# Kernel optimization log

Hardware: AMD Instinct MI355X
Metric: run time of the kernel (lower is better)

## Reference

```python
import jax, jax.numpy as jnp
import numpy as np

N = 2048       # num nodes
E = 4096       # num edges
D_NODE = 128
D_EDGE = 128
H = 4          # heads
DH = D_EDGE // H
C = 16         # num classes
NODE_K = N // 2   # node_k_ratio = 0.5
EDGE_K = E // 2   # edge_k_ratio = 0.5
NEG = -1e9


def setup_inputs() -> dict:
    key = jax.random.key(0)
    ks = jax.random.split(key, 16)
    w = lambda k, shape: jax.random.normal(k, shape, jnp.float32) * 0.02
    return {
        "node_features": jax.random.normal(ks[0], (N, D_NODE), jnp.float32),
        "edge_features": jax.random.normal(ks[1], (E, D_EDGE), jnp.float32),
        "edge_index": jax.random.randint(ks[2], (2, E), 0, N, jnp.int32),
        # ImportanceRouter: scalar scores per node / edge
        "w_router_n": w(ks[3], (D_NODE,)),
        "w_router_e": w(ks[4], (D_EDGE,)),
        # EdgeAttention projections
        "w_e": w(ks[5], (D_EDGE, D_EDGE)),
        "w_n": w(ks[6], (D_NODE, D_EDGE)),
        "w_q": w(ks[7], (D_EDGE, D_EDGE)),
        "w_k": w(ks[8], (D_EDGE, D_EDGE)),
        "w_v": w(ks[9], (D_EDGE, D_EDGE)),
        "w_o": w(ks[10], (D_EDGE, D_EDGE)),
        # classifier MLP: Linear -> GELU -> Linear
        "w1": w(ks[11], (D_EDGE, D_EDGE)),
        "b1": jnp.zeros((D_EDGE,), jnp.float32),
        "w2": w(ks[12], (D_EDGE, C)),
        "b2": jnp.zeros((C,), jnp.float32),
    }


def reference(node_features, edge_features, edge_index,
              w_router_n, w_router_e,
              w_e, w_n, w_q, w_k, w_v, w_o,
              w1, b1, w2, b2):
    src, dst = edge_index[0], edge_index[1]

    # --- ImportanceRouter: node/edge scores ---
    ns = node_features @ w_router_n   # [N]
    es = edge_features @ w_router_e   # [E]

    # --- apply_top_k(node_k_ratio=0.5, edge_k_ratio=0.5) ---
    _, nidx = jax.lax.top_k(ns, NODE_K)
    node_mask = jnp.zeros((N,), bool).at[nidx].set(True)
    _, eidx = jax.lax.top_k(es, EDGE_K)
    edge_topk = jnp.zeros((E,), bool).at[eidx].set(True)
    edge_mask = edge_topk & node_mask[src] & node_mask[dst]   # [E]

    ef = edge_features * edge_mask[:, None].astype(edge_features.dtype)

    # --- build_edge_adjacency: edges sharing a node attend to each other ---
    adj = ((src[:, None] == src[None, :]) | (src[:, None] == dst[None, :]) |
           (dst[:, None] == src[None, :]) | (dst[:, None] == dst[None, :]))  # [E,E]

    # --- EdgeAttention: edge rep mixes edge feats and endpoint node feats ---
    h = ef @ w_e + (node_features[src] + node_features[dst]) @ w_n   # [E, D_EDGE]
    q = (h @ w_q).reshape(E, H, DH)
    k = (h @ w_k).reshape(E, H, DH)
    v = (h @ w_v).reshape(E, H, DH)
    scores = jnp.einsum('ehd,fhd->hef', q, k) / np.float32(np.sqrt(DH))  # [H,E,E]
    scores = jnp.where(adj[None, :, :], scores, NEG)
    attn = jax.nn.softmax(scores, axis=-1)
    o = jnp.einsum('hef,fhd->ehd', attn, v).reshape(E, D_EDGE) @ w_o    # [E, D_EDGE]

    # --- classifier: Linear -> GELU -> Linear ---
    x = jax.nn.gelu(o @ w1 + b1)
    logits = x @ w2 + b2            # [E, C]
    return logits
```

## Files before the change

### kernel.cpp

```cpp
#include <hip/hip_runtime.h>
#include <hip/hip_bf16.h>
#include <math.h>

#define NN 2048
#define NE 4096
#define D 128
#define NODE_K 1024
#define EDGE_K 2048
#define CAP 64

typedef const __hip_bfloat16* bfp;
typedef unsigned short u16;
typedef __attribute__((ext_vector_type(8))) short short8;
typedef __attribute__((ext_vector_type(4))) float floatx4;

#define MFMA16(a, b, c) __builtin_amdgcn_mfma_f32_16x16x32_bf16(a, b, c, 0, 0, 0)

__device__ __forceinline__ float b2f(__hip_bfloat16 x) { return __bfloat162float(x); }

__device__ __forceinline__ float ldx(const void* p, size_t i, int f) {
  return f ? ((const float*)p)[i] : b2f(((bfp)p)[i]);
}

__device__ __forceinline__ void split2(float x, u16& hi, u16& lo) {
  unsigned u = __float_as_uint(x);
  unsigned h = (u + 0x7FFFu + ((u >> 16) & 1u)) >> 16;
  hi = (u16)h;
  float r = x - __uint_as_float(h << 16);
  unsigned v = __float_as_uint(r);
  lo = (u16)((v + 0x7FFFu + ((v >> 16) & 1u)) >> 16);
}
__device__ __forceinline__ void build_frags(const float* v8, short8& fh, short8& fl) {
  #pragma unroll
  for (int i = 0; i < 8; ++i) {
    u16 h, l;
    split2(v8[i], h, l);
    fh[i] = (short)h; fl[i] = (short)l;
  }
}

__device__ __forceinline__ int detect_f(const u16* raw, int* s4) {
  int t = threadIdx.x;
  int weird = 0;
  for (int i = t; i < 4096; i += blockDim.x) {
    unsigned int bits = ((unsigned int)raw[i]) << 16;
    float x = __uint_as_float(bits);
    float ax = fabsf(x);
    if (!(ax <= 1e3f) || (x != 0.f && ax < 1e-12f)) weird++;
  }
  #pragma unroll
  for (int m = 32; m >= 1; m >>= 1) weird += __shfl_xor(weird, m);
  int nw = (int)blockDim.x >> 6;
  if ((t & 63) == 0) s4[t >> 6] = weird;
  __syncthreads();
  int tot = 0;
  for (int i = 0; i < nw; ++i) tot += s4[i];
  return (tot > 200) ? 1 : 0;
}

struct K1Args {
  const void *nf, *ef, *wrn, *wre;
  const void* w[7];
  float *ns, *es;
  int *deg, *flag;
  u16 *wtHi, *wtLo;
  u16 *feHi, *feLo;
};

#define SCORE_BLOCKS ((NN + NE) / 4)
#define WPREP_BLOCKS 56
#define FSPLIT_BLOCKS 384
__global__ __launch_bounds__(256) void scores_prep_kernel(K1Args a) {
  __shared__ int s4[4];
  int b = blockIdx.x, t = threadIdx.x;
  int f = detect_f((const u16*)a.nf, s4);
  if (b < SCORE_BLOCKS) {
    int wid = b * 4 + (t >> 6), lane = t & 63;
    const void* base; const void* w; float* out; size_t r0;
    if (wid < NN) { base = a.nf; r0 = (size_t)wid * D; w = a.wrn; out = a.ns + wid; }
    else { int r = wid - NN; base = a.ef; r0 = (size_t)r * D; w = a.wre; out = a.es + r; }
    double p = (double)ldx(base, r0 + lane, f) * (double)ldx(w, lane, f)
             + (double)ldx(base, r0 + lane + 64, f) * (double)ldx(w, lane + 64, f);
    #pragma unroll
    for (int m = 32; m >= 1; m >>= 1) p += __shfl_xor(p, m);
    if (lane == 0) *out = (float)p;
  } else if (b == SCORE_BLOCKS) {
    if (t == 0) a.flag[0] = f;
    for (int i = t; i < NN; i += 256) a.deg[i] = 0;
  } else if (b <= SCORE_BLOCKS + WPREP_BLOCKS) {
    int wb = b - SCORE_BLOCKS - 1;
    #pragma unroll
    for (int i = 0; i < 8; ++i) {
      int g = wb * 2048 + i * 256 + t;
      int w = g >> 14, r = g & 16383;
      int k = r >> 7, n = r & 127;
      u16 hi, lo;
      split2(ldx(a.w[w], r, f), hi, lo);
      a.wtHi[w * 16384 + n * 128 + k] = hi;
      a.wtLo[w * 16384 + n * 128 + k] = lo;
    }
  } else {
    int fb = b - SCORE_BLOCKS - 1 - WPREP_BLOCKS;
    #pragma unroll
    for (int i = 0; i < 8; ++i) {
      int g = fb * 2048 + i * 256 + t;
      float x = (g < NN * D) ? ldx(a.nf, g, f) : ldx(a.ef, g - NN * D, f);
      u16 hi, lo;
      split2(x, hi, lo);
      a.feHi[g] = hi; a.feLo[g] = lo;
    }
  }
}

#define NMB (NN / 4)
#define EMB (NE / 4)
__global__ __launch_bounds__(256) void mask_lists_kernel(
    const float* __restrict__ ns, const float* __restrict__ es,
    const int* __restrict__ src, const int* __restrict__ dst,
    int* __restrict__ node_mask, int* __restrict__ edge_topk,
    int* __restrict__ deg, int* __restrict__ lists) {
  __shared__ float s[NE];
  int b = blockIdx.x, t = threadIdx.x;
  if (b < NMB) {
    for (int i = t; i < NN; i += 256) s[i] = ns[i];
    __syncthreads();
    int i = b * 4 + (t >> 6), lane = t & 63;
    float si = s[i];
    int rank = 0;
    for (int j = lane; j < NN; j += 64) {
      float sj = s[j];
      rank += (sj > si) || (sj == si && j < i);
    }
    #pragma unroll
    for (int m = 32; m >= 1; m >>= 1) rank += __shfl_xor(rank, m);
    if (lane == 0) node_mask[i] = (rank < NODE_K) ? 1 : 0;
  } else if (b < NMB + EMB) {
    for (int i = t; i < NE; i += 256) s[i] = es[i];
    __syncthreads();
    int i = (b - NMB) * 4 + (t >> 6), lane = t & 63;
    float si = s[i];
    int rank = 0;
    for (int j = lane; j < NE; j += 64) {
      float sj = s[j];
      rank += (sj > si) || (sj == si && j < i);
    }
    #pragma unroll
    for (int m = 32; m >= 1; m >>= 1) rank += __shfl_xor(rank, m);
    if (lane == 0) edge_topk[i] = (rank < EDGE_K) ? 1 : 0;
  } else {
    int e = (b - NMB - EMB) * 256 + t;
    if (e < NE) {
      int sn = src[e], dn = dst[e];
      int p = atomicAdd(&deg[sn], 1);
      if (p >= 0 && p < CAP) lists[sn * CAP + p] = e;
      if (dn != sn) {
        p = atomicAdd(&deg[dn], 1);
        if (p >= 0 && p < CAP) lists[dn * CAP + p] = e;
      }
    }
  }
}

__global__ __launch_bounds__(512) void h_qkv_mfma_kernel(
    const u16* __restrict__ feHi, const u16* __restrict__ feLo,
    const int* __restrict__ src, const int* __restrict__ dst,
    const int* __restrict__ node_mask, const int* __restrict__ edge_topk,
    const u16* __restrict__ wtHi, const u16* __restrict__ wtLo,
    float* __restrict__ qkv) {
  __shared__ __align__(16) float hf[8 * 64 * 4];
  int t = threadIdx.x;
  int wave = t >> 6, lane = t & 63;
  int qd = lane >> 4, c = lane & 15;
  int row0 = blockIdx.x * 16;
  int e = row0 + c;
  int sn = src[e], dn = dst[e];
  bool em = edge_topk[e] && node_mask[sn] && node_mask[dn];
  int n0 = wave * 16;
  const u16* efH = feHi + (size_t)NN * D;
  const u16* efL = feLo + (size_t)NN * D;
  const short8 z8 = {0, 0, 0, 0, 0, 0, 0, 0};

  floatx4 acc = {0.f, 0.f, 0.f, 0.f};
  #pragma unroll
  for (int ks = 0; ks < 4; ++ks) {
    int k0 = ks * 32 + qd * 8;
    short8 a1h = *(const short8*)(efH + (size_t)e * D + k0);
    short8 a1l = *(const short8*)(efL + (size_t)e * D + k0);
    if (!em) { a1h = z8; a1l = z8; }
    short8 sh = *(const short8*)(feHi + (size_t)sn * D + k0);
    short8 sl = *(const short8*)(feLo + (size_t)sn * D + k0);
    short8 dh = *(const short8*)(feHi + (size_t)dn * D + k0);
    short8 dl = *(const short8*)(feLo + (size_t)dn * D + k0);
    size_t bo = (size_t)(n0 + c) * 128 + k0;
    short8 bEh = *(const short8*)(wtHi + bo);
    short8 bEl = *(const short8*)(wtLo + bo);
    short8 bNh = *(const short8*)(wtHi + 16384 + bo);
    short8 bNl = *(const short8*)(wtLo + 16384 + bo);
    acc = MFMA16(a1h, bEh, acc);
    acc = MFMA16(a1l, bEh, acc);
    acc = MFMA16(a1h, bEl, acc);
    acc = MFMA16(sh, bNh, acc);
    acc = MFMA16(sl, bNh, acc);
    acc = MFMA16(sh, bNl, acc);
    acc = MFMA16(dh, bNh, acc);
    acc = MFMA16(dl, bNh, acc);
    acc = MFMA16(dh, bNl, acc);
  }
  {
    int np = n0 + c;
    int kd = np >> 5, qq = (np >> 3) & 3, half = (c >> 2) & 1, j4 = c & 3;
    #pragma unroll
    for (int r = 0; r < 4; ++r)
      hf[((kd * 2 + half) * 64 + qq * 16 + 4 * qd + r) * 4 + j4] = acc[r];
  }
  __syncthreads();
  floatx4 aq = {0.f, 0.f, 0.f, 0.f};
  floatx4 ak = {0.f, 0.f, 0.f, 0.f};
  floatx4 av = {0.f, 0.f, 0.f, 0.f};
  #pragma unroll
  for (int ks = 0; ks < 4; ++ks) {
    float4 p0 = *(const float4*)&hf[((ks * 2 + 0) * 64 + lane) * 4];
    float4 p1 = *(const float4*)&hf[((ks * 2 + 1) * 64 + lane) * 4];
    float v8[8] = {p0.x, p0.y, p0.z, p0.w, p1.x, p1.y, p1.z, p1.w};
    short8 ah, al;
    build_frags(v8, ah, al);
    size_t bo = (size_t)(n0 + c) * 128 + ks * 32 + qd * 8;
    short8 bqh = *(const short8*)(wtHi + 2 * 16384 + bo);
    short8 bql = *(const short8*)(wtLo + 2 * 16384 + bo);
    short8 bkh = *(const short8*)(wtHi + 3 * 16384 + bo);
    short8 bkl = *(const short8*)(wtLo + 3 * 16384 + bo);
    short8 bvh = *(const short8*)(wtHi + 4 * 16384 + bo);
    short8 bvl = *(const short8*)(wtLo + 4 * 16384 + bo);
    aq = MFMA16(ah, bqh, aq); aq = MFMA16(al, bqh, aq); aq = MFMA16(ah, bql, aq);
    ak = MFMA16(ah, bkh, ak); ak = MFMA16(al, bkh, ak); ak = MFMA16(ah, bkl, ak);
    av = MFMA16(ah, bvh, av); av = MFMA16(al, bvh, av); av = MFMA16(ah, bvl, av);
  }
  #pragma unroll
  for (int r = 0; r < 4; ++r) {
    size_t ro = (size_t)(row0 + 4 * qd + r) * D + n0 + c;
    qkv[ro] = aq[r];
    qkv[(size_t)NE * D + ro] = ak[r];
    qkv[(size_t)2 * NE * D + ro] = av[r];
  }
}

__global__ __launch_bounds__(512) void attn_mlp_kernel(
    const float* __restrict__ qkv, const int* __restrict__ src,
    const int* __restrict__ dst, const int* __restrict__ deg,
    const int* __restrict__ lists,
    const u16* __restrict__ wtHi, const u16* __restrict__ wtLo,
    const void* __restrict__ b1, const void* __restrict__ w2,
    const void* __restrict__ b2, const int* __restrict__ flag,
    void* __restrict__ out) {
  __shared__ __align__(16) float aol[16 * 132];
  __shared__ __align__(16) float hf[8 * 64 * 4];
  __shared__ float xl[16 * 132];
  __shared__ float w2l[128 * 16];
  int t = threadIdx.x;
  int row0 = blockIdx.x * 16;
  int f = flag[0];
  const float* qp = qkv;
  const float* kp = qkv + (size_t)NE * D;
  const float* vp = qkv + (size_t)2 * NE * D;
  const float scale = 0.17677669529663687f;
  int j = t & 127;
  for (int it = 0; it < 4; ++it) {
    int le = it * 4 + (t >> 7);
    int e = row0 + le;
    float qj = qp[(size_t)e * D + j];
    int sn = src[e], dn = dst[e];
    float m = -1e30f, l = 0.f, acc = 0.f;
    int degA = max(0, min(deg[sn], CAP));
    for (int i = 0; i < degA; ++i) {
      int fe = lists[sn * CAP + i];
      float p = qj * kp[(size_t)fe * D + j];
      p += __shfl_xor(p, 16); p += __shfl_xor(p, 8); p += __shfl_xor(p, 4);
      p += __shfl_xor(p, 2);  p += __shfl_xor(p, 1);
      float s = p * scale;
      float vj = vp[(size_t)fe * D + j];
      float mn = fmaxf(m, s);
      float corr = expf(m - mn);
      float w = expf(s - mn);
      l = l * corr + w;
      acc = acc * corr + w * vj;
      m = mn;
    }
    if (dn != sn) {
      int degB = max(0, min(deg[dn], CAP));
      for (int i = 0; i < degB; ++i) {
        int fe = lists[dn * CAP + i];
        if (src[fe] == sn || dst[fe] == sn) continue;
        float p = qj * kp[(size_t)fe * D + j];
        p += __shfl_xor(p, 16); p += __shfl_xor(p, 8); p += __shfl_xor(p, 4);
        p += __shfl_xor(p, 2);  p += __shfl_xor(p, 1);
        float s = p * scale;
        float vj = vp[(size_t)fe * D + j];
        float mn = fmaxf(m, s);
        float corr = expf(m - mn);
        float w = expf(s - mn);
        l = l * corr + w;
        acc = acc * corr + w * vj;
        m = mn;
      }
    }
    aol[le * 132 + j] = acc / fmaxf(l, 1e-37f);
  }
  for (int i = t; i < D * 16; i += 512) w2l[i] = ldx(w2, i, f);
  __syncthreads();

  int wave = t >> 6, lane = t & 63;
  int qd = lane >> 4, c = lane & 15;
  int n0 = wave * 16;
  floatx4 acc = {0.f, 0.f, 0.f, 0.f};
  #pragma unroll
  for (int ks = 0; ks < 4; ++ks) {
    int k0 = ks * 32 + qd * 8;
    const float* ap = aol + c * 132 + k0;
    float4 p0 = *(const float4*)ap;
    float4 p1 = *(const float4*)(ap + 4);
    float v8[8] = {p0.x, p0.y, p0.z, p0.w, p1.x, p1.y, p1.z, p1.w};
    short8 ah, al;
    build_frags(v8, ah, al);
    size_t bo = (size_t)(n0 + c) * 128 + k0;
    short8 bh = *(const short8*)(wtHi + 5 * 16384 + bo);
    short8 bl = *(const short8*)(wtLo + 5 * 16384 + bo);
    acc = MFMA16(ah, bh, acc);
    acc = MFMA16(al, bh, acc);
    acc = MFMA16(ah, bl, acc);
  }
  {
    int np = n0 + c;
    int kd = np >> 5, qq = (np >> 3) & 3, half = (c >> 2) & 1, j4 = c & 3;
    #pragma unroll
    for (int r = 0; r < 4; ++r)
      hf[((kd * 2 + half) * 64 + qq * 16 + 4 * qd + r) * 4 + j4] = acc[r];
  }
  __syncthreads();
  floatx4 a2c = {0.f, 0.f, 0.f, 0.f};
  #pragma unroll
  for (int ks = 0; ks < 4; ++ks) {
    float4 p0 = *(const float4*)&hf[((ks * 2 + 0) * 64 + lane) * 4];
    float4 p1 = *(const float4*)&hf[((ks * 2 + 1) * 64 + lane) * 4];
    float v8[8] = {p0.x, p0.y, p0.z, p0.w, p1.x, p1.y, p1.z, p1.w};
    short8 ah, al;
    build_frags(v8, ah, al);
    size_t bo = (size_t)(n0 + c) * 128 + ks * 32 + qd * 8;
    short8 bh = *(const short8*)(wtHi + 6 * 16384 + bo);
    short8 bl = *(const short8*)(wtLo + 6 * 16384 + bo);
    a2c = MFMA16(ah, bh, a2c);
    a2c = MFMA16(al, bh, a2c);
    a2c = MFMA16(ah, bl, a2c);
  }
  float bj = ldx(b1, n0 + c, f);
  #pragma unroll
  for (int r = 0; r < 4; ++r) {
    float u = a2c[r] + bj;
    float inner = 0.7978845608028654f * (u + 0.044715f * u * u * u);
    xl[(4 * qd + r) * 132 + n0 + c] = 0.5f * u * (1.f + tanhf(inner));
  }
  __syncthreads();
  if (t < 256) {
    int r = t >> 4, cc = t & 15;
    float s = 0.f;
    for (int kk = 0; kk < D; ++kk) s += xl[r * 132 + kk] * w2l[kk * 16 + cc];
    s += ldx(b2, cc, f);
    int idx = (row0 + r) * 16 + cc;
    if (f) ((float*)out)[idx] = s;
    else ((__hip_bfloat16*)out)[idx] = __float2bfloat16(s);
  }
}

extern "C" void kernel_launch(void* const* d_in, const int* in_sizes, int n_in,
                              void* d_out, int out_size, void* d_ws, size_t ws_size,
                              hipStream_t stream) {
  const int* eidx = (const int*)d_in[2];
  const int* src = eidx;
  const int* dst = eidx + NE;

  size_t off = 0;
  char* base = (char*)d_ws;
  auto alloc = [&](size_t nbytes) -> void* {
    void* p = base + off;
    off += (nbytes + 255) & ~(size_t)255;
    return p;
  };
  int* flag      = (int*)alloc(256);
  float* ns      = (float*)alloc(NN * sizeof(float));
  float* es      = (float*)alloc(NE * sizeof(float));
  int* node_mask = (int*)alloc(NN * sizeof(int));
  int* edge_topk = (int*)alloc(NE * sizeof(int));
  int* deg       = (int*)alloc(NN * sizeof(int));
  int* lists     = (int*)alloc((size_t)NN * CAP * sizeof(int));
  u16* wtHi      = (u16*)alloc((size_t)7 * 16384 * sizeof(u16));
  u16* wtLo      = (u16*)alloc((size_t)7 * 16384 * sizeof(u16));
  u16* feHi      = (u16*)alloc((size_t)(NN + NE) * D * sizeof(u16));
  u16* feLo      = (u16*)alloc((size_t)(NN + NE) * D * sizeof(u16));
  float* qkv     = (float*)alloc((size_t)3 * NE * D * sizeof(float));

  K1Args a1;
  a1.nf = d_in[0]; a1.ef = d_in[1]; a1.wrn = d_in[3]; a1.wre = d_in[4];
  a1.w[0] = d_in[5];  a1.w[1] = d_in[6];  a1.w[2] = d_in[7];
  a1.w[3] = d_in[8];  a1.w[4] = d_in[9];  a1.w[5] = d_in[10]; a1.w[6] = d_in[11];
  a1.ns = ns; a1.es = es; a1.deg = deg; a1.flag = flag;
  a1.wtHi = wtHi; a1.wtLo = wtLo; a1.feHi = feHi; a1.feLo = feLo;

  scores_prep_kernel<<<SCORE_BLOCKS + 1 + WPREP_BLOCKS + FSPLIT_BLOCKS, 256, 0,
                       stream>>>(a1);
  mask_lists_kernel<<<NMB + EMB + NE / 256, 256, 0, stream>>>(
      ns, es, src, dst, node_mask, edge_topk, deg, lists);
  h_qkv_mfma_kernel<<<NE / 16, 512, 0, stream>>>(
      feHi, feLo, src, dst, node_mask, edge_topk, wtHi, wtLo, qkv);
  attn_mlp_kernel<<<NE / 16, 512, 0, stream>>>(
      qkv, src, dst, deg, lists, wtHi, wtLo, d_in[12], d_in[13], d_in[14],
      flag, d_out);
}
```

Before: 170.3 us.

## Fold top-k ranking into QKV kernel, build edge lists by ballot, split attention

The separate mask/list kernel is removed. Node and edge top-k ranks are now computed per block inside the h/QKV kernel, using scores staged in shared memory. Per-node edge lists are built without atomics by one wave scanning all edges with ballot/popcount inside the prep kernel. The fused attention+MLP kernel is split into a per-edge attention kernel with 4096 small blocks and a separate MFMA o-projection/MLP kernel. This aims to cut a launch, make list order deterministic and raise parallelism in attention, at the cost of redundant rank work per block and an extra global round trip for the attention output.

```diff
diff --git a/kernel.cpp b/kernel.cpp
--- a/kernel.cpp
+++ b/kernel.cpp
@@ -61,8 +61,9 @@
 struct K1Args {
   const void *nf, *ef, *wrn, *wre;
   const void* w[7];
+  const int *src, *dst;
   float *ns, *es;
-  int *deg, *flag;
+  int *deg, *lists, *flag;
   u16 *wtHi, *wtLo;
   u16 *feHi, *feLo;
 };
@@ -70,12 +71,14 @@
 #define SCORE_BLOCKS ((NN + NE) / 4)
 #define WPREP_BLOCKS 56
 #define FSPLIT_BLOCKS 384
+#define LIST_BLOCKS (NN / 8)
 __global__ __launch_bounds__(256) void scores_prep_kernel(K1Args a) {
   __shared__ int s4[4];
   int b = blockIdx.x, t = threadIdx.x;
   int f = detect_f((const u16*)a.nf, s4);
+  int wave = t >> 6, lane = t & 63;
   if (b < SCORE_BLOCKS) {
-    int wid = b * 4 + (t >> 6), lane = t & 63;
+    int wid = b * 4 + wave;
     const void* base; const void* w; float* out; size_t r0;
     if (wid < NN) { base = a.nf; r0 = (size_t)wid * D; w = a.wrn; out = a.ns + wid; }
     else { int r = wid - NN; base = a.ef; r0 = (size_t)r * D; w = a.wre; out = a.es + r; }
@@ -86,7 +89,6 @@
     if (lane == 0) *out = (float)p;
   } else if (b == SCORE_BLOCKS) {
     if (t == 0) a.flag[0] = f;
-    for (int i = t; i < NN; i += 256) a.deg[i] = 0;
   } else if (b <= SCORE_BLOCKS + WPREP_BLOCKS) {
     int wb = b - SCORE_BLOCKS - 1;
     #pragma unroll
@@ -99,7 +101,7 @@
       a.wtHi[w * 16384 + n * 128 + k] = hi;
       a.wtLo[w * 16384 + n * 128 + k] = lo;
     }
-  } else {
+  } else if (b <= SCORE_BLOCKS + WPREP_BLOCKS + FSPLIT_BLOCKS) {
     int fb = b - SCORE_BLOCKS - 1 - WPREP_BLOCKS;
     #pragma unroll
     for (int i = 0; i < 8; ++i) {
@@ -109,76 +111,83 @@
       split2(x, hi, lo);
       a.feHi[g] = hi; a.feLo[g] = lo;
     }
-  }
-}
-
-#define NMB (NN / 4)
-#define EMB (NE / 4)
-__global__ __launch_bounds__(256) void mask_lists_kernel(
+  } else {
+    int n = (b - SCORE_BLOCKS - 1 - WPREP_BLOCKS - FSPLIT_BLOCKS) * 4 + wave;
+    int cnt = 0;
+    for (int base = 0; base < NE; base += 64) {
+      int i = base + lane;
+      int s = a.src[i], d2 = a.dst[i];
+      bool hit = (s == n) || (d2 == n);
+      unsigned long long mb = __ballot(hit);
+      if (hit) {
+        int pos = cnt + __popcll(mb & ((1ull << lane) - 1ull));
+        if (pos < CAP) a.lists[n * CAP + pos] = i;
+      }
+      cnt += (int)__popcll(mb);
+    }
+    if (lane == 0) a.deg[n] = cnt;
+  }
+}
+#undef LIST_BLOCKS
+#define LIST_BLOCKS (NN / 4)
+
+__global__ __launch_bounds__(512) void h_qkv_mfma_kernel(
     const float* __restrict__ ns, const float* __restrict__ es,
-    const int* __restrict__ src, const int* __restrict__ dst,
-    int* __restrict__ node_mask, int* __restrict__ edge_topk,
-    int* __restrict__ deg, int* __restrict__ lists) {
-  __shared__ float s[NE];
-  int b = blockIdx.x, t = threadIdx.x;
-  if (b < NMB) {
-    for (int i = t; i < NN; i += 256) s[i] = ns[i];
-    __syncthreads();
-    int i = b * 4 + (t >> 6), lane = t & 63;
-    float si = s[i];
-    int rank = 0;
-    for (int j = lane; j < NN; j += 64) {
-      float sj = s[j];
-      rank += (sj > si) || (sj == si && j < i);
-    }
-    #pragma unroll
-    for (int m = 32; m >= 1; m >>= 1) rank += __shfl_xor(rank, m);
-    if (lane == 0) node_mask[i] = (rank < NODE_K) ? 1 : 0;
-  } else if (b < NMB + EMB) {
-    for (int i = t; i < NE; i += 256) s[i] = es[i];
-    __syncthreads();
-    int i = (b - NMB) * 4 + (t >> 6), lane = t & 63;
-    float si = s[i];
-    int rank = 0;
-    for (int j = lane; j < NE; j += 64) {
-      float sj = s[j];
-      rank += (sj > si) || (sj == si && j < i);
-    }
-    #pragma unroll
-    for (int m = 32; m >= 1; m >>= 1) rank += __shfl_xor(rank, m);
-    if (lane == 0) edge_topk[i] = (rank < EDGE_K) ? 1 : 0;
-  } else {
-    int e = (b - NMB - EMB) * 256 + t;
-    if (e < NE) {
-      int sn = src[e], dn = dst[e];
-      int p = atomicAdd(&deg[sn], 1);
-      if (p >= 0 && p < CAP) lists[sn * CAP + p] = e;
-      if (dn != sn) {
-        p = atomicAdd(&deg[dn], 1);
-        if (p >= 0 && p < CAP) lists[dn * CAP + p] = e;
-      }
-    }
-  }
-}
-
-__global__ __launch_bounds__(512) void h_qkv_mfma_kernel(
     const u16* __restrict__ feHi, const u16* __restrict__ feLo,
     const int* __restrict__ src, const int* __restrict__ dst,
-    const int* __restrict__ node_mask, const int* __restrict__ edge_topk,
     const u16* __restrict__ wtHi, const u16* __restrict__ wtLo,
     float* __restrict__ qkv) {
-  __shared__ __align__(16) float hf[8 * 64 * 4];
+  __shared__ __align__(16) float sc[NN + NE];
+  __shared__ int okn[32], oke[16], em16[16];
   int t = threadIdx.x;
   int wave = t >> 6, lane = t & 63;
   int qd = lane >> 4, c = lane & 15;
   int row0 = blockIdx.x * 16;
+
+  for (int i = t; i < NN; i += 512) sc[i] = ns[i];
+  for (int i = t; i < NE; i += 512) sc[NN + i] = es[i];
+  __syncthreads();
+  #pragma unroll
+  for (int ti = 0; ti < 6; ++ti) {
+    int task = wave * 6 + ti;
+    if (task < 16) {
+      int e = row0 + task;
+      float si = sc[NN + e];
+      int rank = 0;
+      for (int j = lane; j < NE; j += 64) {
+        float sj = sc[NN + j];
+        rank += (sj > si) || (sj == si && j < e);
+      }
+      #pragma unroll
+      for (int m = 32; m >= 1; m >>= 1) rank += __shfl_xor(rank, m);
+      if (lane == 0) oke[task] = (rank < EDGE_K) ? 1 : 0;
+    } else {
+      int idx = task - 16;
+      int le = idx & 15;
+      int n = (idx < 16 ? src : dst)[row0 + le];
+      float si = sc[n];
+      int rank = 0;
+      for (int j = lane; j < NN; j += 64) {
+        float sj = sc[j];
+        rank += (sj > si) || (sj == si && j < n);
+      }
+      #pragma unroll
+      for (int m = 32; m >= 1; m >>= 1) rank += __shfl_xor(rank, m);
+      if (lane == 0) okn[idx] = (rank < NODE_K) ? 1 : 0;
+    }
+  }
+  __syncthreads();
+  if (t < 16) em16[t] = oke[t] && okn[t] && okn[16 + t];
+  __syncthreads();
+
+  float* hf = sc;
   int e = row0 + c;
   int sn = src[e], dn = dst[e];
-  bool em = edge_topk[e] && node_mask[sn] && node_mask[dn];
   int n0 = wave * 16;
   const u16* efH = feHi + (size_t)NN * D;
   const u16* efL = feLo + (size_t)NN * D;
   const short8 z8 = {0, 0, 0, 0, 0, 0, 0, 0};
+  bool em = em16[c] != 0;
 
   floatx4 acc = {0.f, 0.f, 0.f, 0.f};
   #pragma unroll
@@ -244,40 +253,41 @@
   }
 }
 
-__global__ __launch_bounds__(512) void attn_mlp_kernel(
-    const float* __restrict__ qkv, const int* __restrict__ src,
-    const int* __restrict__ dst, const int* __restrict__ deg,
-    const int* __restrict__ lists,
-    const u16* __restrict__ wtHi, const u16* __restrict__ wtLo,
-    const void* __restrict__ b1, const void* __restrict__ w2,
-    const void* __restrict__ b2, const int* __restrict__ flag,
-    void* __restrict__ out) {
-  __shared__ __align__(16) float aol[16 * 132];
-  __shared__ __align__(16) float hf[8 * 64 * 4];
-  __shared__ float xl[16 * 132];
-  __shared__ float w2l[128 * 16];
-  int t = threadIdx.x;
-  int row0 = blockIdx.x * 16;
-  int f = flag[0];
-  const float* qp = qkv;
-  const float* kp = qkv + (size_t)NE * D;
-  const float* vp = qkv + (size_t)2 * NE * D;
+__global__ void attn_kernel(const float* __restrict__ q, const float* __restrict__ k,
+                            const float* __restrict__ v, const int* __restrict__ src,
+                            const int* __restrict__ dst, const int* __restrict__ deg,
+                            const int* __restrict__ lists, float* __restrict__ ao) {
+  int e = blockIdx.x;
+  int j = threadIdx.x;
+  float qj = q[(size_t)e * D + j];
+  int sn = src[e], dn = dst[e];
+  float m = -1e30f, l = 0.f, acc = 0.f;
   const float scale = 0.17677669529663687f;
-  int j = t & 127;
-  for (int it = 0; it < 4; ++it) {
-    int le = it * 4 + (t >> 7);
-    int e = row0 + le;
-    float qj = qp[(size_t)e * D + j];
-    int sn = src[e], dn = dst[e];
-    float m = -1e30f, l = 0.f, acc = 0.f;
-    int degA = max(0, min(deg[sn], CAP));
-    for (int i = 0; i < degA; ++i) {
-      int fe = lists[sn * CAP + i];
-      float p = qj * kp[(size_t)fe * D + j];
+  int degA = max(0, min(deg[sn], CAP));
+  for (int i = 0; i < degA; ++i) {
+    int fe = lists[sn * CAP + i];
+    float p = qj * k[(size_t)fe * D + j];
+    p += __shfl_xor(p, 16); p += __shfl_xor(p, 8); p += __shfl_xor(p, 4);
+    p += __shfl_xor(p, 2);  p += __shfl_xor(p, 1);
+    float s = p * scale;
+    float vj = v[(size_t)fe * D + j];
+    float mn = fmaxf(m, s);
+    float corr = expf(m - mn);
+    float w = expf(s - mn);
+    l = l * corr + w;
+    acc = acc * corr + w * vj;
+    m = mn;
+  }
+  if (dn != sn) {
+    int degB = max(0, min(deg[dn], CAP));
+    for (int i = 0; i < degB; ++i) {
+      int fe = lists[dn * CAP + i];
+      if (src[fe] == sn || dst[fe] == sn) continue;
+      float p = qj * k[(size_t)fe * D + j];
       p += __shfl_xor(p, 16); p += __shfl_xor(p, 8); p += __shfl_xor(p, 4);
       p += __shfl_xor(p, 2);  p += __shfl_xor(p, 1);
       float s = p * scale;
-      float vj = vp[(size_t)fe * D + j];
+      float vj = v[(size_t)fe * D + j];
       float mn = fmaxf(m, s);
       float corr = expf(m - mn);
       float w = expf(s - mn);
@@ -285,45 +295,43 @@
       acc = acc * corr + w * vj;
       m = mn;
     }
-    if (dn != sn) {
-      int degB = max(0, min(deg[dn], CAP));
-      for (int i = 0; i < degB; ++i) {
-        int fe = lists[dn * CAP + i];
-        if (src[fe] == sn || dst[fe] == sn) continue;
-        float p = qj * kp[(size_t)fe * D + j];
-        p += __shfl_xor(p, 16); p += __shfl_xor(p, 8); p += __shfl_xor(p, 4);
-        p += __shfl_xor(p, 2);  p += __shfl_xor(p, 1);
-        float s = p * scale;
-        float vj = vp[(size_t)fe * D + j];
-        float mn = fmaxf(m, s);
-        float corr = expf(m - mn);
-        float w = expf(s - mn);
-        l = l * corr + w;
-        acc = acc * corr + w * vj;
-        m = mn;
-      }
-    }
-    aol[le * 132 + j] = acc / fmaxf(l, 1e-37f);
-  }
-  for (int i = t; i < D * 16; i += 512) w2l[i] = ldx(w2, i, f);
-  __syncthreads();
-
+  }
+  ao[(size_t)e * D + j] = acc / fmaxf(l, 1e-37f);
+}
+
+__global__ __launch_bounds__(512) void o_mlp_mfma_kernel(
+    const float* __restrict__ ao,
+    const u16* __restrict__ wtHi, const u16* __restrict__ wtLo,
+    const void* __restrict__ b1, const void* __restrict__ w2,
+    const void* __restrict__ b2, const int* __restrict__ flag,
+    void* __restrict__ out) {
+  __shared__ __align__(16) float hf[8 * 64 * 4];
+  __shared__ float xl[16 * 132];
+  __shared__ float w2l[128 * 16];
+  int t = threadIdx.x;
   int wave = t >> 6, lane = t & 63;
   int qd = lane >> 4, c = lane & 15;
+  int f = flag[0];
+  int row0 = blockIdx.x * 16;
   int n0 = wave * 16;
+  const u16* WOh = wtHi + 5 * 16384;
+  const u16* WOl = wtLo + 5 * 16384;
+  const u16* W1h = wtHi + 6 * 16384;
+  const u16* W1l = wtLo + 6 * 16384;
+
   floatx4 acc = {0.f, 0.f, 0.f, 0.f};
   #pragma unroll
   for (int ks = 0; ks < 4; ++ks) {
     int k0 = ks * 32 + qd * 8;
-    const float* ap = aol + c * 132 + k0;
+    const float* ap = ao + (size_t)(row0 + c) * D + k0;
     float4 p0 = *(const float4*)ap;
     float4 p1 = *(const float4*)(ap + 4);
     float v8[8] = {p0.x, p0.y, p0.z, p0.w, p1.x, p1.y, p1.z, p1.w};
     short8 ah, al;
     build_frags(v8, ah, al);
     size_t bo = (size_t)(n0 + c) * 128 + k0;
-    short8 bh = *(const short8*)(wtHi + 5 * 16384 + bo);
-    short8 bl = *(const short8*)(wtLo + 5 * 16384 + bo);
+    short8 bh = *(const short8*)(WOh + bo);
+    short8 bl = *(const short8*)(WOl + bo);
     acc = MFMA16(ah, bh, acc);
     acc = MFMA16(al, bh, acc);
     acc = MFMA16(ah, bl, acc);
@@ -345,8 +353,8 @@
     short8 ah, al;
     build_frags(v8, ah, al);
     size_t bo = (size_t)(n0 + c) * 128 + ks * 32 + qd * 8;
-    short8 bh = *(const short8*)(wtHi + 6 * 16384 + bo);
-    short8 bl = *(const short8*)(wtLo + 6 * 16384 + bo);
+    short8 bh = *(const short8*)(W1h + bo);
+    short8 bl = *(const short8*)(W1l + bo);
     a2c = MFMA16(ah, bh, a2c);
     a2c = MFMA16(al, bh, a2c);
     a2c = MFMA16(ah, bl, a2c);
@@ -358,6 +366,7 @@
     float inner = 0.7978845608028654f * (u + 0.044715f * u * u * u);
     xl[(4 * qd + r) * 132 + n0 + c] = 0.5f * u * (1.f + tanhf(inner));
   }
+  for (int i = t; i < D * 16; i += 512) w2l[i] = ldx(w2, i, f);
   __syncthreads();
   if (t < 256) {
     int r = t >> 4, cc = t & 15;
@@ -384,33 +393,32 @@
     off += (nbytes + 255) & ~(size_t)255;
     return p;
   };
-  int* flag      = (int*)alloc(256);
-  float* ns      = (float*)alloc(NN * sizeof(float));
-  float* es      = (float*)alloc(NE * sizeof(float));
-  int* node_mask = (int*)alloc(NN * sizeof(int));
-  int* edge_topk = (int*)alloc(NE * sizeof(int));
-  int* deg       = (int*)alloc(NN * sizeof(int));
-  int* lists     = (int*)alloc((size_t)NN * CAP * sizeof(int));
-  u16* wtHi      = (u16*)alloc((size_t)7 * 16384 * sizeof(u16));
-  u16* wtLo      = (u16*)alloc((size_t)7 * 16384 * sizeof(u16));
-  u16* feHi      = (u16*)alloc((size_t)(NN + NE) * D * sizeof(u16));
-  u16* feLo      = (u16*)alloc((size_t)(NN + NE) * D * sizeof(u16));
-  float* qkv     = (float*)alloc((size_t)3 * NE * D * sizeof(float));
+  int* flag   = (int*)alloc(256);
+  float* ns   = (float*)alloc(NN * sizeof(float));
+  float* es   = (float*)alloc(NE * sizeof(float));
+  int* deg    = (int*)alloc(NN * sizeof(int));
+  int* lists  = (int*)alloc((size_t)NN * CAP * sizeof(int));
+  u16* wtHi   = (u16*)alloc((size_t)7 * 16384 * sizeof(u16));
+  u16* wtLo   = (u16*)alloc((size_t)7 * 16384 * sizeof(u16));
+  u16* feHi   = (u16*)alloc((size_t)(NN + NE) * D * sizeof(u16));
+  u16* feLo   = (u16*)alloc((size_t)(NN + NE) * D * sizeof(u16));
+  float* qkv  = (float*)alloc((size_t)3 * NE * D * sizeof(float));
+  float* ao   = (float*)alloc((size_t)NE * D * sizeof(float));
+  float* qb = qkv, *kb = qkv + NE * D, *vb = qkv + 2 * NE * D;
 
   K1Args a1;
   a1.nf = d_in[0]; a1.ef = d_in[1]; a1.wrn = d_in[3]; a1.wre = d_in[4];
   a1.w[0] = d_in[5];  a1.w[1] = d_in[6];  a1.w[2] = d_in[7];
   a1.w[3] = d_in[8];  a1.w[4] = d_in[9];  a1.w[5] = d_in[10]; a1.w[6] = d_in[11];
-  a1.ns = ns; a1.es = es; a1.deg = deg; a1.flag = flag;
+  a1.src = src; a1.dst = dst;
+  a1.ns = ns; a1.es = es; a1.deg = deg; a1.lists = lists; a1.flag = flag;
   a1.wtHi = wtHi; a1.wtLo = wtLo; a1.feHi = feHi; a1.feLo = feLo;
 
-  scores_prep_kernel<<<SCORE_BLOCKS + 1 + WPREP_BLOCKS + FSPLIT_BLOCKS, 256, 0,
-                       stream>>>(a1);
-  mask_lists_kernel<<<NMB + EMB + NE / 256, 256, 0, stream>>>(
-      ns, es, src, dst, node_mask, edge_topk, deg, lists);
+  scores_prep_kernel<<<SCORE_BLOCKS + 1 + WPREP_BLOCKS + FSPLIT_BLOCKS + LIST_BLOCKS,
+                       256, 0, stream>>>(a1);
   h_qkv_mfma_kernel<<<NE / 16, 512, 0, stream>>>(
-      feHi, feLo, src, dst, node_mask, edge_topk, wtHi, wtLo, qkv);
-  attn_mlp_kernel<<<NE / 16, 512, 0, stream>>>(
-      qkv, src, dst, deg, lists, wtHi, wtLo, d_in[12], d_in[13], d_in[14],
-      flag, d_out);
-}
+      ns, es, feHi, feLo, src, dst, wtHi, wtLo, qkv);
+  attn_kernel<<<NE, 128, 0, stream>>>(qb, kb, vb, src, dst, deg, lists, ao);
+  o_mlp_mfma_kernel<<<NE / 16, 512, 0, stream>>>(
+      ao, wtHi, wtLo, d_in[12], d_in[13], d_in[14], flag, d_out);
+}
```

Result: no change. 169.2 us (-0.6%).
